# Kernel optimization log

Hardware: AMD Instinct MI355X
Metric: run time of the kernel (lower is better)

The kernel has to match this reference:

```python
import jax, jax.numpy as jnp
import numpy as np

# group boundaries (start with 0), ragged sizes cycling 16/32/48/64
_SIZES = np.tile(np.array([16, 32, 48, 64], dtype=np.int64), 16)  # 64 groups
GROUP = np.concatenate([[0], np.cumsum(_SIZES)])                   # [65]
SEG_IDS = np.repeat(np.arange(len(_SIZES)), _SIZES)                # [T=2560]
N_GROUPS = len(_SIZES)
D0 = 128  # also the attention scale (module divides by d0, NOT sqrt(d0))
B, T = 256, int(GROUP[-1])


def setup_inputs() -> dict:
    key = jax.random.key(0)
    k1, k2 = jax.random.split(key)
    s_i = jax.random.normal(k1, (B, D0), dtype=jnp.float32)
    theta_i = jax.random.normal(k2, (B, T, D0), dtype=jnp.float32)
    return {"s_i": s_i, "theta_i": theta_i}


def reference(s_i, theta_i):
    # Fused ragged attention over all groups: q_len == 1 per group.
    seg = jnp.asarray(SEG_IDS)                                   # [T]
    # scores u[b,t] = <s_i[b], theta_i[b,t]> / d0
    u = jnp.einsum('bd,btd->bt', s_i, theta_i) / D0              # [B,T]
    ut = u.T                                                     # [T,B] (segment ops over leading axis)
    m = jax.ops.segment_max(ut, seg, num_segments=N_GROUPS)      # [G,B]
    e = jnp.exp(ut - m[seg])                                     # [T,B]
    denom = jax.ops.segment_sum(e, seg, num_segments=N_GROUPS)   # [G,B]
    attn = e / denom[seg]                                        # [T,B] per-group softmax
    # out[b,g,d] = sum_{t in group g} attn[t,b] * theta_i[b,t,d]
    w = attn[:, :, None] * theta_i.transpose(1, 0, 2)            # [T,B,D]
    out = jax.ops.segment_sum(w, seg, num_segments=N_GROUPS)     # [G,B,D]
    return out.transpose(1, 0, 2)                                # [B,G,D]
```

## Files before the change

kernel.cpp:

```cpp
#include <hip/hip_runtime.h>
#include <math.h>

constexpr int D = 128;
constexpr int B = 256;
constexpr int T = 2560;
constexpr int G = 64;

__global__ __launch_bounds__(256) void ragged_attn_kernel(
    const float* __restrict__ s_i,
    const float* __restrict__ theta,
    float* __restrict__ out)
{
    const int g = blockIdx.x;
    const int b = blockIdx.y;

    const int gm = g & 3;
    const int S  = 16 * (gm + 1);
    const int t0 = (g >> 2) * 160 + (gm * (gm + 1) / 2) * 16;

    __shared__ float4 lds_tile4[64 * 32];
    __shared__ float  u_sh[64];
    __shared__ float  attn_sh[64];
    __shared__ float  partial[128];

    const int tid = threadIdx.x;
    const int c = tid & 31;
    const int r = tid >> 5;

    const float4 s4 = ((const float4*)(s_i + (size_t)b * D))[c];

    const float4* theta4 = (const float4*)(theta + ((size_t)b * T + t0) * D);

    const int passes = S >> 3;
    for (int p = 0; p < passes; ++p) {
        const int t = p * 8 + r;
        const float4 th = theta4[t * 32 + c];
        lds_tile4[t * 32 + c] = th;
        float dot = th.x * s4.x + th.y * s4.y + th.z * s4.z + th.w * s4.w;
        #pragma unroll
        for (int m = 16; m >= 1; m >>= 1) dot += __shfl_xor(dot, m);
        if (c == 0) u_sh[t] = dot * (1.0f / 128.0f);
    }
    __syncthreads();

    if (tid < 64) {
        const float v = (tid < S) ? u_sh[tid] : -INFINITY;
        float mx = v;
        #pragma unroll
        for (int m = 32; m >= 1; m >>= 1) mx = fmaxf(mx, __shfl_xor(mx, m));
        const float e = (tid < S) ? __expf(v - mx) : 0.0f;
        float sum = e;
        #pragma unroll
        for (int m = 32; m >= 1; m >>= 1) sum += __shfl_xor(sum, m);
        attn_sh[tid] = e / sum;
    }
    __syncthreads();

    const float* tile = (const float*)lds_tile4;
    const int d    = tid & 127;
    const int half = tid >> 7;
    const int half_rows = S >> 1;
    const int tstart = half * half_rows;
    float acc = 0.0f;
    for (int t = 0; t < half_rows; ++t) {
        const int tt = tstart + t;
        acc += attn_sh[tt] * tile[tt * 128 + d];
    }
    if (half == 1) partial[d] = acc;
    __syncthreads();
    if (half == 0) {
        out[((size_t)b * G + g) * D + d] = acc + partial[d];
    }
}

extern "C" void kernel_launch(void* const* d_in, const int* in_sizes, int n_in,
                              void* d_out, int out_size, void* d_ws, size_t ws_size,
                              hipStream_t stream) {
    const float* s_i   = (const float*)d_in[0];
    const float* theta = (const float*)d_in[1];
    float* out = (float*)d_out;

    dim3 grid(G, B);
    ragged_attn_kernel<<<grid, 256, 0, stream>>>(s_i, theta, out);
}
```

Measured before the change: 478.3 us.

## Use online softmax over 32-row chunks to halve LDS tile and raise occupancy

Replaces the single 64-row LDS tile with a 32-row chunked loop that keeps a running max and sum (online softmax) and rescales the accumulator per chunk. This halves shared memory per block and requests 8 blocks per CU via launch bounds, aiming to hide global load latency with more resident blocks. Loads are also paired two rows per iteration. In exchange, 64-row groups need two chunks, adding extra barriers and an exp rescale per chunk.

```diff
diff --git a/kernel.cpp b/kernel.cpp
--- a/kernel.cpp
+++ b/kernel.cpp
@@ -6,7 +6,7 @@
 constexpr int T = 2560;
 constexpr int G = 64;
 
-__global__ __launch_bounds__(256) void ragged_attn_kernel(
+__global__ __launch_bounds__(256, 8) void ragged_attn_kernel(
     const float* __restrict__ s_i,
     const float* __restrict__ theta,
     float* __restrict__ out)
@@ -18,58 +18,90 @@
     const int S  = 16 * (gm + 1);
     const int t0 = (g >> 2) * 160 + (gm * (gm + 1) / 2) * 16;
 
-    __shared__ float4 lds_tile4[64 * 32];
-    __shared__ float  u_sh[64];
-    __shared__ float  attn_sh[64];
+    __shared__ float4 lds_tile4[32 * 32];
+    __shared__ float  u_sh[32];
+    __shared__ float  e_sh[64];
     __shared__ float  partial[128];
+    __shared__ float  m_sh, l_sh, alpha_sh;
 
     const int tid = threadIdx.x;
     const int c = tid & 31;
     const int r = tid >> 5;
+    const int d    = tid & 127;
+    const int half = tid >> 7;
 
     const float4 s4 = ((const float4*)(s_i + (size_t)b * D))[c];
+    const float4* theta4 = (const float4*)(theta + ((size_t)b * T + t0) * D);
+    const float* tile = (const float*)lds_tile4;
 
-    const float4* theta4 = (const float4*)(theta + ((size_t)b * T + t0) * D);
-
-    const int passes = S >> 3;
-    for (int p = 0; p < passes; ++p) {
-        const int t = p * 8 + r;
-        const float4 th = theta4[t * 32 + c];
-        lds_tile4[t * 32 + c] = th;
-        float dot = th.x * s4.x + th.y * s4.y + th.z * s4.z + th.w * s4.w;
-        #pragma unroll
-        for (int m = 16; m >= 1; m >>= 1) dot += __shfl_xor(dot, m);
-        if (c == 0) u_sh[t] = dot * (1.0f / 128.0f);
-    }
+    if (tid == 0) { m_sh = -INFINITY; l_sh = 0.0f; }
     __syncthreads();
 
-    if (tid < 64) {
-        const float v = (tid < S) ? u_sh[tid] : -INFINITY;
-        float mx = v;
-        #pragma unroll
-        for (int m = 32; m >= 1; m >>= 1) mx = fmaxf(mx, __shfl_xor(mx, m));
-        const float e = (tid < S) ? __expf(v - mx) : 0.0f;
-        float sum = e;
-        #pragma unroll
-        for (int m = 32; m >= 1; m >>= 1) sum += __shfl_xor(sum, m);
-        attn_sh[tid] = e / sum;
+    float acc = 0.0f;
+
+    for (int t_off = 0; t_off < S; t_off += 32) {
+        const int cr = min(32, S - t_off);
+        const int passes = cr >> 3;
+
+        for (int p = 0; p < passes; p += 2) {
+            const int ta = p * 8 + r;
+            const int tb = ta + 8;
+            const float4 a0 = theta4[(size_t)(t_off + ta) * 32 + c];
+            const float4 a1 = theta4[(size_t)(t_off + tb) * 32 + c];
+            lds_tile4[ta * 32 + c] = a0;
+            lds_tile4[tb * 32 + c] = a1;
+            float d0v = a0.x * s4.x + a0.y * s4.y + a0.z * s4.z + a0.w * s4.w;
+            float d1v = a1.x * s4.x + a1.y * s4.y + a1.z * s4.z + a1.w * s4.w;
+            #pragma unroll
+            for (int m = 16; m >= 1; m >>= 1) {
+                d0v += __shfl_xor(d0v, m);
+                d1v += __shfl_xor(d1v, m);
+            }
+            if (c == 0) {
+                u_sh[ta] = d0v * (1.0f / 128.0f);
+                u_sh[tb] = d1v * (1.0f / 128.0f);
+            }
+        }
+        __syncthreads();
+
+        if (tid < 64) {
+            const float m_old = m_sh;
+            const float v = (tid < cr) ? u_sh[tid] : -INFINITY;
+            float cm = v;
+            #pragma unroll
+            for (int m = 32; m >= 1; m >>= 1) cm = fmaxf(cm, __shfl_xor(cm, m));
+            const float m_new = fmaxf(m_old, cm);
+            const float e = (tid < cr) ? __expf(v - m_new) : 0.0f;
+            float sum = e;
+            #pragma unroll
+            for (int m = 32; m >= 1; m >>= 1) sum += __shfl_xor(sum, m);
+            e_sh[tid] = e;
+            if (tid == 0) {
+                const float alpha = __expf(m_old - m_new);
+                alpha_sh = alpha;
+                l_sh = l_sh * alpha + sum;
+                m_sh = m_new;
+            }
+        }
+        __syncthreads();
+
+        const float alpha = alpha_sh;
+        const int hr = cr >> 1;
+        const int tstart = half * hr;
+        float a = 0.0f;
+        for (int j = 0; j < hr; ++j) {
+            const int tt = tstart + j;
+            a += e_sh[tt] * tile[tt * 128 + d];
+        }
+        acc = acc * alpha + a;
+        __syncthreads();
     }
-    __syncthreads();
 
-    const float* tile = (const float*)lds_tile4;
-    const int d    = tid & 127;
-    const int half = tid >> 7;
-    const int half_rows = S >> 1;
-    const int tstart = half * half_rows;
-    float acc = 0.0f;
-    for (int t = 0; t < half_rows; ++t) {
-        const int tt = tstart + t;
-        acc += attn_sh[tt] * tile[tt * 128 + d];
-    }
+    const float l = l_sh;
     if (half == 1) partial[d] = acc;
     __syncthreads();
     if (half == 0) {
-        out[((size_t)b * G + g) * D + d] = acc + partial[d];
+        out[((size_t)b * G + g) * D + d] = (acc + partial[d]) / l;
     }
 }
 
```

Result: faster. 451.7 us (-5.6%).

## Assign one wavefront per group with streaming online softmax and register prefetch

Applied to the files above, without the earlier changes.

Each group is now handled by one 64-lane wavefront instead of a whole 256-thread block, with four groups packed per block. Theta is processed in 8-row chunks using an online-softmax recurrence, and the next chunk is prefetched into registers while the current one is consumed. This removes block-wide __syncthreads and cuts LDS from a full 64-row tile down to a small per-wave staging buffer, which should raise occupancy and hide memory latency in this bandwidth-bound kernel. The cost is extra exp/rescale work per chunk. There is also load imbalance, because the four waves in a block handle groups of 16, 32, 48 and 64 rows.

```diff
diff --git a/kernel.cpp b/kernel.cpp
--- a/kernel.cpp
+++ b/kernel.cpp
@@ -5,72 +5,91 @@
 constexpr int B = 256;
 constexpr int T = 2560;
 constexpr int G = 64;
+constexpr int R = 8;
 
-__global__ __launch_bounds__(256) void ragged_attn_kernel(
+__global__ __launch_bounds__(256, 8) void ragged_attn_wave(
     const float* __restrict__ s_i,
     const float* __restrict__ theta,
     float* __restrict__ out)
 {
-    const int g = blockIdx.x;
-    const int b = blockIdx.y;
+    const int w    = threadIdx.x >> 6;
+    const int lane = threadIdx.x & 63;
+    const int q    = blockIdx.x & 15;
+    const int b    = blockIdx.x >> 4;
+    const int g    = q * 4 + w;
+    const int gm   = g & 3;
+    const int S    = 16 * (gm + 1);
+    const int t0   = (g >> 2) * 160 + (gm * (gm + 1) / 2) * 16;
 
-    const int gm = g & 3;
-    const int S  = 16 * (gm + 1);
-    const int t0 = (g >> 2) * 160 + (gm * (gm + 1) / 2) * 16;
+    __shared__ float tile[4][R * 128];
+    __shared__ float u_sh[4][R];
 
-    __shared__ float4 lds_tile4[64 * 32];
-    __shared__ float  u_sh[64];
-    __shared__ float  attn_sh[64];
-    __shared__ float  partial[128];
-
-    const int tid = threadIdx.x;
-    const int c = tid & 31;
-    const int r = tid >> 5;
+    const int h = lane >> 5;
+    const int c = lane & 31;
 
     const float4 s4 = ((const float4*)(s_i + (size_t)b * D))[c];
-
     const float4* theta4 = (const float4*)(theta + ((size_t)b * T + t0) * D);
 
-    const int passes = S >> 3;
-    for (int p = 0; p < passes; ++p) {
-        const int t = p * 8 + r;
-        const float4 th = theta4[t * 32 + c];
-        lds_tile4[t * 32 + c] = th;
-        float dot = th.x * s4.x + th.y * s4.y + th.z * s4.z + th.w * s4.w;
+    float m = -INFINITY, l = 0.0f;
+    float acc0 = 0.0f, acc1 = 0.0f;
+    const int nch = S >> 3;
+
+    float4 rb[4];
+    #pragma unroll
+    for (int k = 0; k < 4; ++k)
+        rb[k] = theta4[(size_t)(2 * k + h) * 32 + c];
+
+    for (int ch = 0; ch < nch; ++ch) {
+        float dt[4];
         #pragma unroll
-        for (int m = 16; m >= 1; m >>= 1) dot += __shfl_xor(dot, m);
-        if (c == 0) u_sh[t] = dot * (1.0f / 128.0f);
+        for (int k = 0; k < 4; ++k) {
+            const float4 v = rb[k];
+            ((float4*)&tile[w][(2 * k + h) * 128])[c] = v;
+            dt[k] = v.x * s4.x + v.y * s4.y + v.z * s4.z + v.w * s4.w;
+        }
+        if (ch + 1 < nch) {
+            #pragma unroll
+            for (int k = 0; k < 4; ++k)
+                rb[k] = theta4[(size_t)((ch + 1) * R + 2 * k + h) * 32 + c];
+        }
+        #pragma unroll
+        for (int k = 0; k < 4; ++k) {
+            #pragma unroll
+            for (int msk = 16; msk >= 1; msk >>= 1)
+                dt[k] += __shfl_xor(dt[k], msk);
+        }
+        if (c == 0) {
+            #pragma unroll
+            for (int k = 0; k < 4; ++k)
+                u_sh[w][2 * k + h] = dt[k] * (1.0f / 128.0f);
+        }
+        float uu[R];
+        float cm = -INFINITY;
+        #pragma unroll
+        for (int t = 0; t < R; ++t) {
+            uu[t] = u_sh[w][t];
+            cm = fmaxf(cm, uu[t]);
+        }
+        const float m_new = fmaxf(m, cm);
+        const float alpha = __expf(m - m_new);
+        acc0 *= alpha;
+        acc1 *= alpha;
+        float se = 0.0f;
+        #pragma unroll
+        for (int t = 0; t < R; ++t) {
+            const float e = __expf(uu[t] - m_new);
+            se += e;
+            acc0 += e * tile[w][t * 128 + lane];
+            acc1 += e * tile[w][t * 128 + 64 + lane];
+        }
+        l = l * alpha + se;
+        m = m_new;
     }
-    __syncthreads();
 
-    if (tid < 64) {
-        const float v = (tid < S) ? u_sh[tid] : -INFINITY;
-        float mx = v;
-        #pragma unroll
-        for (int m = 32; m >= 1; m >>= 1) mx = fmaxf(mx, __shfl_xor(mx, m));
-        const float e = (tid < S) ? __expf(v - mx) : 0.0f;
-        float sum = e;
-        #pragma unroll
-        for (int m = 32; m >= 1; m >>= 1) sum += __shfl_xor(sum, m);
-        attn_sh[tid] = e / sum;
-    }
-    __syncthreads();
-
-    const float* tile = (const float*)lds_tile4;
-    const int d    = tid & 127;
-    const int half = tid >> 7;
-    const int half_rows = S >> 1;
-    const int tstart = half * half_rows;
-    float acc = 0.0f;
-    for (int t = 0; t < half_rows; ++t) {
-        const int tt = tstart + t;
-        acc += attn_sh[tt] * tile[tt * 128 + d];
-    }
-    if (half == 1) partial[d] = acc;
-    __syncthreads();
-    if (half == 0) {
-        out[((size_t)b * G + g) * D + d] = acc + partial[d];
-    }
+    float* op = out + ((size_t)b * G + g) * D;
+    const float inv_l = 1.0f / l;
+    op[lane]      = acc0 * inv_l;
+    op[lane + 64] = acc1 * inv_l;
 }
 
 extern "C" void kernel_launch(void* const* d_in, const int* in_sizes, int n_in,
@@ -80,6 +99,5 @@
     const float* theta = (const float*)d_in[1];
     float* out = (float*)d_out;
 
-    dim3 grid(G, B);
-    ragged_attn_kernel<<<grid, 256, 0, stream>>>(s_i, theta, out);
+    ragged_attn_wave<<<dim3(B * 16), 256, 0, stream>>>(s_i, theta, out);
 }
```

Result: faster. 448.1 us (-6.3%).
